# Performance work log

Measured on AMD Instinct MI355X. Metric: run time of the kernel, lower is better.

Reference implementation:

```python
import jax, jax.numpy as jnp
import numpy as np

B, S, D = 4, 4096, 1024
H, WIN = 16, 256
DK = D // H
NW = S // WIN


def setup_inputs() -> dict:
    key = jax.random.key(0)
    ks = jax.random.split(key, 11)
    mk = lambda k, shape: jax.random.normal(k, shape, dtype=jnp.float32)
    w = lambda k: mk(k, (D, D)) * 0.02  # torch Linear weight [out, in]
    b = lambda k: mk(k, (D,)) * 0.02
    return {
        "query": mk(ks[0], (B, S, D)),
        "key": mk(ks[1], (B, S, D)),
        "value": mk(ks[2], (B, S, D)),
        "Wq": w(ks[3]), "bq": b(ks[4]),
        "Wk": w(ks[5]), "bk": b(ks[6]),
        "Wv": w(ks[7]), "bv": b(ks[8]),
        "Wo": w(ks[9]), "bo": b(ks[10]),
    }


def reference(query, key, value, Wq, bq, Wk, bk, Wv, bv, Wo, bo):
    scale = 1.0 / float(DK) ** 0.5

    def proj(x, Wm, bi):
        y = x @ Wm.T + bi
        return y.reshape(B, S, H, DK).transpose(0, 2, 1, 3).reshape(B, H, NW, WIN, DK)

    q = proj(query, Wq, bq)
    k = proj(key, Wk, bk)
    v = proj(value, Wv, bv)

    scores = jnp.einsum("bhnqd,bhnkd->bhnqk", q, k) * scale
    p_attn = jax.nn.softmax(scores, axis=-1)
    x = jnp.einsum("bhnqk,bhnkd->bhnqd", p_attn, v)

    # merge windows + heads -> [B,S,D], then output projection
    x = x.reshape(B, H, S, DK).transpose(0, 2, 1, 3).reshape(B, S, D)
    return x @ Wo.T + bo
```

## Files before the change

### kernel.cpp

```cpp
#include <hip/hip_runtime.h>
#include <hip/hip_bf16.h>

typedef __attribute__((ext_vector_type(8))) __bf16 bf16x8;
typedef __attribute__((ext_vector_type(4))) float f32x4;

#define DEVI static __device__ __forceinline__


DEVI ushort f2bf(float f) {
  unsigned u = __builtin_bit_cast(unsigned, f);
  return (ushort)((u + 0x7fffu + ((u >> 16) & 1u)) >> 16);
}

union BF8 { unsigned u[4]; bf16x8 v; };

DEVI bf16x8 cvt8(const float* __restrict__ p) {
  const f32x4 a = *(const f32x4*)p;
  const f32x4 b = *(const f32x4*)(p + 4);
  BF8 r;
  asm("v_cvt_pk_bf16_f32 %0, %1, %2" : "=v"(r.u[0]) : "v"(a.x), "v"(a.y));
  asm("v_cvt_pk_bf16_f32 %0, %1, %2" : "=v"(r.u[1]) : "v"(a.z), "v"(a.w));
  asm("v_cvt_pk_bf16_f32 %0, %1, %2" : "=v"(r.u[2]) : "v"(b.x), "v"(b.y));
  asm("v_cvt_pk_bf16_f32 %0, %1, %2" : "=v"(r.u[3]) : "v"(b.z), "v"(b.w));
  return r.v;
}

DEVI bf16x8 cvt8r(f32x4 a, f32x4 b) {
  BF8 r;
  asm("v_cvt_pk_bf16_f32 %0, %1, %2" : "=v"(r.u[0]) : "v"(a.x), "v"(a.y));
  asm("v_cvt_pk_bf16_f32 %0, %1, %2" : "=v"(r.u[1]) : "v"(a.z), "v"(a.w));
  asm("v_cvt_pk_bf16_f32 %0, %1, %2" : "=v"(r.u[2]) : "v"(b.x), "v"(b.y));
  asm("v_cvt_pk_bf16_f32 %0, %1, %2" : "=v"(r.u[3]) : "v"(b.z), "v"(b.w));
  return r.v;
}

DEVI void gload16(const void* g, void* l) {
  __builtin_amdgcn_global_load_lds(
      (const __attribute__((address_space(1))) unsigned*)g,
      (__attribute__((address_space(3))) unsigned*)l, 16, 0, 0);
}

DEVI int xcd_swizzle(int bid, int nwg) {
  return (bid & 7) * (nwg >> 3) + (bid >> 3);
}

DEVI f32x4 mfma16(bf16x8 a, bf16x8 b, f32x4 c) {
  return __builtin_amdgcn_mfma_f32_16x16x32_bf16(a, b, c, 0, 0, 0);
}


__global__ __launch_bounds__(256) void cvt_qkv(
    const float* __restrict__ q, const float* __restrict__ k,
    const float* __restrict__ v, ushort* __restrict__ oq,
    ushort* __restrict__ ok2, ushort* __restrict__ ov) {
  const int s = blockIdx.x >> 10;
  const int tb = blockIdx.x & 1023;
  const float* src = s == 0 ? q : (s == 1 ? k : v);
  ushort* dst = s == 0 ? oq : (s == 1 ? ok2 : ov);
  const size_t base = (size_t)tb * 2048 + threadIdx.x;

  f32x4 va[8], vb[8];
#pragma unroll
  for (int j = 0; j < 8; ++j) {
    const float* p = src + (base + j * 256) * 8;
    va[j] = __builtin_nontemporal_load((const f32x4*)p);
    vb[j] = __builtin_nontemporal_load((const f32x4*)(p + 4));
  }
#pragma unroll
  for (int j = 0; j < 8; ++j)
    *(bf16x8*)(dst + (base + j * 256) * 8) = cvt8r(va[j], vb[j]);
}

__global__ __launch_bounds__(256) void cvt_w(
    const float* __restrict__ wq, const float* __restrict__ wk,
    const float* __restrict__ wv, const float* __restrict__ wo,
    ushort* __restrict__ oq, ushort* __restrict__ ok2,
    ushort* __restrict__ ov, ushort* __restrict__ oo) {
  const int s = blockIdx.x >> 7;
  const int tb = blockIdx.x & 127;
  const float* src = s == 0 ? wq : (s == 1 ? wk : (s == 2 ? wv : wo));
  ushort* dst = s == 0 ? oq : (s == 1 ? ok2 : (s == 2 ? ov : oo));
  const unsigned G = 128 * 256;
  const unsigned t = tb * 256 + threadIdx.x;
#pragma unroll
  for (int j = 0; j < 4; ++j) {
    const size_t i = (size_t)t + (size_t)j * G;
    *(bf16x8*)(dst + i * 8) = cvt8(src + i * 8);
  }
}


template <int OUT>
__global__ __launch_bounds__(512, 2) void gemm_8ph(
    const ushort* __restrict__ A, const ushort* __restrict__ B,
    const float* __restrict__ bias, void* __restrict__ Cp, int N, int K) {
  __shared__ __align__(16) ushort Asm[4][8192];
  __shared__ __align__(16) ushort Bsm[4][8192];
  const int tid = threadIdx.x, lane = tid & 63;
  const int wv = tid >> 6;
  const int wr = wv >> 2, wc = wv & 3;
  const int cc = lane & 15, cr = lane >> 4;
  const int nw = N >> 8;
  const int work = xcd_swizzle(blockIdx.x, gridDim.x);
  const size_t m0 = (size_t)(work / nw) * 256;
  const size_t n0 = (size_t)(work % nw) * 256;

  const ushort *ag[2], *bg[2];
#pragma unroll
  for (int h = 0; h < 2; ++h) {
    const int u = tid + h * 512;
    const int row = u >> 2, slot = u & 3;
    const int gc = (slot ^ ((row >> 1) & 3)) * 8;
    ag[h] = A + (m0 + row) * (size_t)K + gc;
    bg[h] = B + (n0 + row) * (size_t)K + gc;
  }

  auto stageh = [&](int buf, int kt, int h) {
    gload16(ag[h] + kt, &Asm[buf][(tid + h * 512) * 8]);
    gload16(bg[h] + kt, &Bsm[buf][(tid + h * 512) * 8]);
  };

  f32x4 acc[8][4] = {};
  const int nt = K >> 5;

  int aoff[8], boff[4];
#pragma unroll
  for (int m = 0; m < 8; ++m) {
    const int row = wr * 128 + m * 16 + cc;
    aoff[m] = (row * 4 + (cr ^ ((row >> 1) & 3))) * 8;
  }
#pragma unroll
  for (int n = 0; n < 4; ++n) {
    const int row = wc * 64 + n * 16 + cc;
    boff[n] = (row * 4 + (cr ^ ((row >> 1) & 3))) * 8;
  }

#pragma unroll
  for (int p = 0; p < 3; ++p) {
    stageh(p, p << 5, 0);
    stageh(p, p << 5, 1);
  }
  asm volatile("s_waitcnt vmcnt(8)" ::: "memory");
  __builtin_amdgcn_s_barrier();
  asm volatile("" ::: "memory");

  for (int k = 0; k < nt; ++k) {
    const ushort* Ab = Asm[k & 3];
    const ushort* Bb = Bsm[k & 3];
    const int wb = (k + 3) & 3;
    const bool more = (k + 3 < nt);
    bf16x8 bf[4], af[4];

#pragma unroll
    for (int n = 0; n < 4; ++n) bf[n] = *(const bf16x8*)&Bb[boff[n]];
#pragma unroll
    for (int m = 0; m < 4; ++m) af[m] = *(const bf16x8*)&Ab[aoff[m]];
    if (more) stageh(wb, (k + 3) << 5, 0);
    __builtin_amdgcn_s_barrier();
    asm volatile("s_waitcnt lgkmcnt(0)" ::: "memory");
    __builtin_amdgcn_s_setprio(1);
#pragma unroll
    for (int m = 0; m < 4; ++m)
#pragma unroll
      for (int n = 0; n < 4; ++n)
        acc[m][n] = mfma16(af[m], bf[n], acc[m][n]);
    __builtin_amdgcn_s_setprio(0);
    asm volatile("" ::: "memory");
    __builtin_amdgcn_s_barrier();

#pragma unroll
    for (int m = 0; m < 4; ++m) af[m] = *(const bf16x8*)&Ab[aoff[4 + m]];
    if (more) stageh(wb, (k + 3) << 5, 1);
    if (k < nt - 3) {
      asm volatile("s_waitcnt vmcnt(8)" ::: "memory");
    } else if (k == nt - 3) {
      asm volatile("s_waitcnt vmcnt(4)" ::: "memory");
    } else if (k == nt - 2) {
      asm volatile("s_waitcnt vmcnt(0)" ::: "memory");
    }
    __builtin_amdgcn_s_barrier();
    asm volatile("s_waitcnt lgkmcnt(0)" ::: "memory");
    __builtin_amdgcn_s_setprio(1);
#pragma unroll
    for (int m = 0; m < 4; ++m)
#pragma unroll
      for (int n = 0; n < 4; ++n)
        acc[4 + m][n] = mfma16(af[m], bf[n], acc[4 + m][n]);
    __builtin_amdgcn_s_setprio(0);
    asm volatile("" ::: "memory");
    __builtin_amdgcn_s_barrier();
  }

#pragma unroll
  for (int n = 0; n < 4; ++n) {
    const size_t col = n0 + wc * 64 + n * 16 + cc;
    const float bval = bias[col];
#pragma unroll
    for (int m = 0; m < 8; ++m) {
      const size_t row0 = m0 + wr * 128 + m * 16 + cr * 4;
#pragma unroll
      for (int r = 0; r < 4; ++r) {
        const float val = acc[m][n][r] + bval;
        if constexpr (OUT == 0)
          ((float*)Cp)[(row0 + r) * N + col] = val;
        else if constexpr (OUT == 1)
          ((ushort*)Cp)[(row0 + r) * N + col] = f2bf(val);
        else
          ((ushort*)Cp)[col * 16384 + row0 + r] = f2bf(val);
      }
    }
  }
}


__global__ __launch_bounds__(512) void attn_kernel(
    const ushort* __restrict__ q, const ushort* __restrict__ k,
    const ushort* __restrict__ vt, ushort* __restrict__ x) {
  __shared__ __align__(16) ushort Ks[256 * 64];
  __shared__ __align__(16) ushort Vt[64 * 256];
  __shared__ ushort Pw[8][16 * 264];
  const int bid = blockIdx.x;
  const int w = bid & 15, h = (bid >> 4) & 15, b = bid >> 8;
  const int tid = threadIdx.x, lane = tid & 63, wv = tid >> 6;
  const int cc = lane & 15, cr = lane >> 4;
  const size_t base = ((size_t)b * 4096 + (size_t)w * 256) * 1024 + h * 64;
  const size_t vbase = ((size_t)h * 64) * 16384 + (size_t)b * 4096 + w * 256;

#pragma unroll
  for (int i = 0; i < 4; ++i) {
    const int u = tid + i * 512;
    const int row = u >> 3, slot = u & 7;
    gload16(k + base + (size_t)row * 1024 + ((slot ^ (row & 7)) << 3),
            &Ks[u * 8]);
  }
#pragma unroll
  for (int i = 0; i < 4; ++i) {
    const int u = tid + i * 512;
    const int dk = u >> 5, slot = u & 31;
    gload16(vt + vbase + (size_t)dk * 16384 + (((slot & 24) | ((slot ^ dk) & 7)) << 3),
            &Vt[u * 8]);
  }
  __syncthreads();

  ushort* Pp = Pw[wv];
  for (int c = 0; c < 2; ++c) {
    const int qrow0 = wv * 32 + c * 16;
    const ushort* qp = q + base + (size_t)(qrow0 + cc) * 1024 + cr * 8;
    const bf16x8 qf0 = *(const bf16x8*)qp;
    const bf16x8 qf1 = *(const bf16x8*)(qp + 32);

    f32x4 sc[16];
#pragma unroll
    for (int cb = 0; cb < 16; ++cb) {
      const int row = cb * 16 + cc;
      const bf16x8 kb0 = *(const bf16x8*)&Ks[row * 64 + ((cr ^ (row & 7)) << 3)];
      const bf16x8 kb1 =
          *(const bf16x8*)&Ks[row * 64 + (((4 + cr) ^ (row & 7)) << 3)];
      f32x4 z = {0.f, 0.f, 0.f, 0.f};
      z = mfma16(qf0, kb0, z);
      z = mfma16(qf1, kb1, z);
      sc[cb] = z;
    }

    float inv[4];
#pragma unroll
    for (int r = 0; r < 4; ++r) {
      float mx = -1e30f;
#pragma unroll
      for (int cb = 0; cb < 16; ++cb) mx = fmaxf(mx, sc[cb][r]);
      mx = fmaxf(mx, __shfl_xor(mx, 1));
      mx = fmaxf(mx, __shfl_xor(mx, 2));
      mx = fmaxf(mx, __shfl_xor(mx, 4));
      mx = fmaxf(mx, __shfl_xor(mx, 8));
      float sum = 0.f;
#pragma unroll
      for (int cb = 0; cb < 16; ++cb) {
        const float p = __expf((sc[cb][r] - mx) * 0.125f);
        sc[cb][r] = p;
        sum += p;
      }
      sum += __shfl_xor(sum, 1);
      sum += __shfl_xor(sum, 2);
      sum += __shfl_xor(sum, 4);
      sum += __shfl_xor(sum, 8);
      inv[r] = 1.f / sum;
    }

#pragma unroll
    for (int r = 0; r < 4; ++r)
#pragma unroll
      for (int cb = 0; cb < 16; ++cb)
        Pp[(cr * 4 + r) * 264 + cb * 16 + cc] = f2bf(sc[cb][r]);

    bf16x8 pf[8];
#pragma unroll
    for (int ks = 0; ks < 8; ++ks)
      pf[ks] = *(const bf16x8*)&Pp[cc * 264 + ks * 32 + cr * 8];
    f32x4 o[4] = {};
#pragma unroll
    for (int db = 0; db < 4; ++db) {
      const int row = db * 16 + cc;
#pragma unroll
      for (int ks = 0; ks < 8; ++ks) {
        const int gu = ks * 4 + cr;
        const int lu = (gu & 24) | ((gu ^ row) & 7);
        const bf16x8 bv = *(const bf16x8*)&Vt[row * 256 + lu * 8];
        o[db] = mfma16(pf[ks], bv, o[db]);
      }
    }

#pragma unroll
    for (int db = 0; db < 4; ++db)
#pragma unroll
      for (int r = 0; r < 4; ++r) {
        const int qr = qrow0 + cr * 4 + r;
        x[base + (size_t)qr * 1024 + db * 16 + cc] = f2bf(o[db][r] * inv[r]);
      }
  }
}


extern "C" void kernel_launch(void* const* d_in, const int* in_sizes, int n_in,
                              void* d_out, int out_size, void* d_ws, size_t ws_size,
                              hipStream_t stream) {
  const float* query = (const float*)d_in[0];
  const float* key_  = (const float*)d_in[1];
  const float* value = (const float*)d_in[2];
  const float* Wq = (const float*)d_in[3];
  const float* bq = (const float*)d_in[4];
  const float* Wk = (const float*)d_in[5];
  const float* bk = (const float*)d_in[6];
  const float* Wv = (const float*)d_in[7];
  const float* bv = (const float*)d_in[8];
  const float* Wo = (const float*)d_in[9];
  const float* bo = (const float*)d_in[10];
  float* out = (float*)d_out;

  const size_t MN = (size_t)16384 * 1024;
  const size_t WN = (size_t)1024 * 1024;
  ushort* qb = (ushort*)d_ws;
  ushort* kb = qb + MN;
  ushort* vb = kb + MN;
  ushort* wqb = vb + MN;
  ushort* wkb = wqb + WN;
  ushort* wvb = wkb + WN;
  ushort* wob = wvb + WN;
  ushort* qp = wob + WN;
  ushort* kp = qp + MN;
  ushort* vtp = kp + MN;

  const dim3 b256(256), b512(512);
  const dim3 ggrid(64 * 4);

  cvt_qkv<<<dim3(3 * 1024), b256, 0, stream>>>(query, key_, value, qb, kb, vb);
  cvt_w<<<dim3(4 * 128), b256, 0, stream>>>(Wq, Wk, Wv, Wo, wqb, wkb, wvb, wob);

  gemm_8ph<1><<<ggrid, b512, 0, stream>>>(qb, wqb, bq, qp, 1024, 1024);
  gemm_8ph<1><<<ggrid, b512, 0, stream>>>(kb, wkb, bk, kp, 1024, 1024);
  gemm_8ph<2><<<ggrid, b512, 0, stream>>>(vb, wvb, bv, vtp, 1024, 1024);

  attn_kernel<<<dim3(1024), b512, 0, stream>>>(qp, kp, vtp, qp );

  gemm_8ph<0><<<ggrid, b512, 0, stream>>>(qp, wob, bo, out, 1024, 1024);
}
```

Measured before the change: 291.5 us.

## Fuse fp32-to-bf16 activation conversion into QKV projection GEMM loads

Removes the separate cvt_qkv pass that converted query/key/value to bf16 in workspace. A new GEMM variant loads fp32 A tiles straight into registers, converts them, and writes bf16 into a 4-deep LDS ring, while B still streams via global_load_lds. This avoids writing and rereading about 100MB of bf16 intermediates, at the cost of register-staged A loads, hand-tuned vmcnt waits and more register pressure. Each GEMM now reads twice as many A bytes (fp32), and A tiles are reloaded by every N-block.

```diff
diff --git a/kernel.cpp b/kernel.cpp
--- a/kernel.cpp
+++ b/kernel.cpp
@@ -48,28 +48,6 @@
   return __builtin_amdgcn_mfma_f32_16x16x32_bf16(a, b, c, 0, 0, 0);
 }
 
-
-__global__ __launch_bounds__(256) void cvt_qkv(
-    const float* __restrict__ q, const float* __restrict__ k,
-    const float* __restrict__ v, ushort* __restrict__ oq,
-    ushort* __restrict__ ok2, ushort* __restrict__ ov) {
-  const int s = blockIdx.x >> 10;
-  const int tb = blockIdx.x & 1023;
-  const float* src = s == 0 ? q : (s == 1 ? k : v);
-  ushort* dst = s == 0 ? oq : (s == 1 ? ok2 : ov);
-  const size_t base = (size_t)tb * 2048 + threadIdx.x;
-
-  f32x4 va[8], vb[8];
-#pragma unroll
-  for (int j = 0; j < 8; ++j) {
-    const float* p = src + (base + j * 256) * 8;
-    va[j] = __builtin_nontemporal_load((const f32x4*)p);
-    vb[j] = __builtin_nontemporal_load((const f32x4*)(p + 4));
-  }
-#pragma unroll
-  for (int j = 0; j < 8; ++j)
-    *(bf16x8*)(dst + (base + j * 256) * 8) = cvt8r(va[j], vb[j]);
-}
 
 __global__ __launch_bounds__(256) void cvt_w(
     const float* __restrict__ wq, const float* __restrict__ wk,
@@ -204,6 +182,157 @@
         if constexpr (OUT == 0)
           ((float*)Cp)[(row0 + r) * N + col] = val;
         else if constexpr (OUT == 1)
+          ((ushort*)Cp)[(row0 + r) * N + col] = f2bf(val);
+        else
+          ((ushort*)Cp)[col * 16384 + row0 + r] = f2bf(val);
+      }
+    }
+  }
+}
+
+
+template <int OUT>
+__global__ __launch_bounds__(512, 2) void gemm_8ph_f32a(
+    const float* __restrict__ A, const ushort* __restrict__ B,
+    const float* __restrict__ bias, void* __restrict__ Cp, int N, int K) {
+  __shared__ __align__(16) ushort Asm[4][8192];
+  __shared__ __align__(16) ushort Bsm[4][8192];
+  const int tid = threadIdx.x, lane = tid & 63;
+  const int wv = tid >> 6;
+  const int wr = wv >> 2, wc = wv & 3;
+  const int cc = lane & 15, cr = lane >> 4;
+  const int nw = N >> 8;
+  const int work = xcd_swizzle(blockIdx.x, gridDim.x);
+  const size_t m0 = (size_t)(work / nw) * 256;
+  const size_t n0 = (size_t)(work % nw) * 256;
+
+  const float *af0, *af1;
+  ushort *al0, *al1;
+  {
+    const int u0 = tid, r0 = u0 >> 2, s0 = u0 & 3;
+    const int u1 = tid + 512, r1 = u1 >> 2, s1 = u1 & 3;
+    af0 = A + (m0 + r0) * (size_t)K + (s0 ^ ((r0 >> 1) & 3)) * 8;
+    af1 = A + (m0 + r1) * (size_t)K + (s1 ^ ((r1 >> 1) & 3)) * 8;
+    al0 = &Asm[0][0] + u0 * 8;
+    al1 = &Asm[0][0] + u1 * 8;
+  }
+  const ushort* bg[2];
+#pragma unroll
+  for (int h = 0; h < 2; ++h) {
+    const int u = tid + h * 512;
+    const int row = u >> 2, slot = u & 3;
+    bg[h] = B + (n0 + row) * (size_t)K + (slot ^ ((row >> 1) & 3)) * 8;
+  }
+
+  f32x4 acc[8][4] = {};
+  const int nt = K >> 5;
+
+  int aoff[8], boff[4];
+#pragma unroll
+  for (int m = 0; m < 8; ++m) {
+    const int row = wr * 128 + m * 16 + cc;
+    aoff[m] = (row * 4 + (cr ^ ((row >> 1) & 3))) * 8;
+  }
+#pragma unroll
+  for (int n = 0; n < 4; ++n) {
+    const int row = wc * 64 + n * 16 + cc;
+    boff[n] = (row * 4 + (cr ^ ((row >> 1) & 3))) * 8;
+  }
+
+  f32x4 sa0, sa1, sa2, sa3, sb0, sb1, sb2, sb3;
+#pragma unroll
+  for (int p = 0; p < 2; ++p) {
+    const int kt = p << 5;
+    sa0 = *(const f32x4*)(af0 + kt);  sa1 = *(const f32x4*)(af0 + kt + 4);
+    sa2 = *(const f32x4*)(af1 + kt);  sa3 = *(const f32x4*)(af1 + kt + 4);
+    *(bf16x8*)(al0 + p * 8192) = cvt8r(sa0, sa1);
+    *(bf16x8*)(al1 + p * 8192) = cvt8r(sa2, sa3);
+  }
+  sa0 = *(const f32x4*)(af0 + 64);  sa1 = *(const f32x4*)(af0 + 68);
+  sa2 = *(const f32x4*)(af1 + 64);  sa3 = *(const f32x4*)(af1 + 68);
+#pragma unroll
+  for (int p = 0; p < 3; ++p) {
+    gload16(bg[0] + (p << 5), &Bsm[p][tid * 8]);
+    gload16(bg[1] + (p << 5), &Bsm[p][(tid + 512) * 8]);
+  }
+  asm volatile("s_waitcnt vmcnt(0) lgkmcnt(0)" ::: "memory");
+  __builtin_amdgcn_s_barrier();
+  asm volatile("" ::: "memory");
+
+#define F32A_TILE(k, W0, W1, W2, W3, L0, L1, L2, L3)                          \
+  {                                                                           \
+    const ushort* Ab = Asm[(k) & 3];                                          \
+    const ushort* Bb = Bsm[(k) & 3];                                          \
+    const int wb = ((k) + 3) & 3;                                             \
+    const bool more = ((k) + 3 < nt);                                         \
+    bf16x8 bf[4], af[4];                                                      \
+    _Pragma("unroll")                                                         \
+    for (int n = 0; n < 4; ++n) bf[n] = *(const bf16x8*)&Bb[boff[n]];         \
+    _Pragma("unroll")                                                         \
+    for (int m = 0; m < 4; ++m) af[m] = *(const bf16x8*)&Ab[aoff[m]];         \
+    if (more) {                                                               \
+      const int kt = ((k) + 3) << 5;                                          \
+      L0 = *(const f32x4*)(af0 + kt);  L1 = *(const f32x4*)(af0 + kt + 4);    \
+      L2 = *(const f32x4*)(af1 + kt);  L3 = *(const f32x4*)(af1 + kt + 4);    \
+      gload16(bg[0] + kt, &Bsm[wb][tid * 8]);                                 \
+    }                                                                         \
+    if ((k) < nt - 3) {                                                       \
+      asm volatile("s_waitcnt vmcnt(17)" ::: "memory");                       \
+    } else if ((k) == nt - 3) {                                               \
+      asm volatile("s_waitcnt vmcnt(12)" ::: "memory");                       \
+    } else if ((k) == nt - 2) {                                               \
+      asm volatile("s_waitcnt vmcnt(6)" ::: "memory");                        \
+    } else {                                                                  \
+      asm volatile("s_waitcnt vmcnt(0)" ::: "memory");                        \
+    }                                                                         \
+    __builtin_amdgcn_s_barrier();                                             \
+    asm volatile("s_waitcnt lgkmcnt(0)" ::: "memory");                        \
+    __builtin_amdgcn_s_setprio(1);                                            \
+    _Pragma("unroll")                                                         \
+    for (int m = 0; m < 4; ++m)                                               \
+      _Pragma("unroll")                                                       \
+      for (int n = 0; n < 4; ++n) acc[m][n] = mfma16(af[m], bf[n], acc[m][n]);\
+    __builtin_amdgcn_s_setprio(0);                                            \
+    asm volatile("" ::: "memory");                                            \
+    __builtin_amdgcn_s_barrier();                                             \
+    _Pragma("unroll")                                                         \
+    for (int m = 0; m < 4; ++m) af[m] = *(const bf16x8*)&Ab[aoff[4 + m]];     \
+    if (more) gload16(bg[1] + (((k) + 3) << 5), &Bsm[wb][(tid + 512) * 8]);   \
+    __builtin_amdgcn_s_barrier();                                             \
+    asm volatile("s_waitcnt lgkmcnt(0)" ::: "memory");                        \
+    __builtin_amdgcn_s_setprio(1);                                            \
+    _Pragma("unroll")                                                         \
+    for (int m = 0; m < 4; ++m)                                               \
+      _Pragma("unroll")                                                       \
+      for (int n = 0; n < 4; ++n)                                             \
+        acc[4 + m][n] = mfma16(af[m], bf[n], acc[4 + m][n]);                  \
+    __builtin_amdgcn_s_setprio(0);                                            \
+    if ((k) + 2 < nt) {       \
+      const int wbuf = ((k) + 2) & 3;                                         \
+      *(bf16x8*)(al0 + wbuf * 8192) = cvt8r(W0, W1);                          \
+      *(bf16x8*)(al1 + wbuf * 8192) = cvt8r(W2, W3);                          \
+    }                                                                         \
+    asm volatile("s_waitcnt lgkmcnt(0)" ::: "memory");                        \
+    __builtin_amdgcn_s_barrier();                                             \
+  }
+
+  for (int kk = 0; kk < nt; kk += 2) {
+    F32A_TILE(kk, sa0, sa1, sa2, sa3, sb0, sb1, sb2, sb3);
+    F32A_TILE(kk + 1, sb0, sb1, sb2, sb3, sa0, sa1, sa2, sa3);
+  }
+#undef F32A_TILE
+
+#pragma unroll
+  for (int n = 0; n < 4; ++n) {
+    const size_t col = n0 + wc * 64 + n * 16 + cc;
+    const float bval = bias[col];
+#pragma unroll
+    for (int m = 0; m < 8; ++m) {
+      const size_t row0 = m0 + wr * 128 + m * 16 + cr * 4;
+#pragma unroll
+      for (int r = 0; r < 4; ++r) {
+        const float val = acc[m][n][r] + bval;
+        if constexpr (OUT == 1)
           ((ushort*)Cp)[(row0 + r) * N + col] = f2bf(val);
         else
           ((ushort*)Cp)[col * 16384 + row0 + r] = f2bf(val);
@@ -338,10 +467,7 @@
 
   const size_t MN = (size_t)16384 * 1024;
   const size_t WN = (size_t)1024 * 1024;
-  ushort* qb = (ushort*)d_ws;
-  ushort* kb = qb + MN;
-  ushort* vb = kb + MN;
-  ushort* wqb = vb + MN;
+  ushort* wqb = (ushort*)d_ws;
   ushort* wkb = wqb + WN;
   ushort* wvb = wkb + WN;
   ushort* wob = wvb + WN;
@@ -352,12 +478,11 @@
   const dim3 b256(256), b512(512);
   const dim3 ggrid(64 * 4);
 
-  cvt_qkv<<<dim3(3 * 1024), b256, 0, stream>>>(query, key_, value, qb, kb, vb);
   cvt_w<<<dim3(4 * 128), b256, 0, stream>>>(Wq, Wk, Wv, Wo, wqb, wkb, wvb, wob);
 
-  gemm_8ph<1><<<ggrid, b512, 0, stream>>>(qb, wqb, bq, qp, 1024, 1024);
-  gemm_8ph<1><<<ggrid, b512, 0, stream>>>(kb, wkb, bk, kp, 1024, 1024);
-  gemm_8ph<2><<<ggrid, b512, 0, stream>>>(vb, wvb, bv, vtp, 1024, 1024);
+  gemm_8ph_f32a<1><<<ggrid, b512, 0, stream>>>(query, wqb, bq, qp, 1024, 1024);
+  gemm_8ph_f32a<1><<<ggrid, b512, 0, stream>>>(key_,  wkb, bk, kp, 1024, 1024);
+  gemm_8ph_f32a<2><<<ggrid, b512, 0, stream>>>(value, wvb, bv, vtp, 1024, 1024);
 
   attn_kernel<<<dim3(1024), b512, 0, stream>>>(qp, kp, vtp, qp );
 
```

Measured after the change: 277.6 us. -4.8%, faster.
